# Performance work log

Measured on AMD Instinct MI355X. Metric: run time of the kernel, lower is better.

## Reference

```python
import jax, jax.numpy as jnp
import numpy as np

H, I, B = 256, 128, 512

def setup_inputs() -> dict:
    key = jax.random.key(0)
    ks = jax.random.split(key, 24)
    n = lambda k, shp, s=1.0: jax.random.normal(k, shp, dtype=jnp.float32) * s
    inp = {
        "x": n(ks[0], (B, I)),
        "hx": n(ks[1], (B, H), 0.1),
        "cx": n(ks[2], (B, H, H), 0.1),
        # input->gate weights (hidden, input), xavier-like scale
        "Wii": n(ks[3], (H, I), (2.0 / (H + I)) ** 0.5),
        "Wif": n(ks[4], (H, I), (2.0 / (H + I)) ** 0.5),
        "Wig": n(ks[5], (H, I), (2.0 / (H + I)) ** 0.5),
        "Wio": n(ks[6], (H, I), (2.0 / (H + I)) ** 0.5),
        # hidden->gate weights (hidden, hidden), ~orthogonal scale
        "Whi": n(ks[7], (H, H), H ** -0.5),
        "Whit": n(ks[8], (H, H), H ** -0.5),
        "Whf": n(ks[9], (H, H), H ** -0.5),
        "Whft": n(ks[10], (H, H), H ** -0.5),
        "Whc": n(ks[11], (H, H), H ** -0.5),
        "Whct": n(ks[12], (H, H), H ** -0.5),
        "Who": n(ks[13], (H, H), H ** -0.5),
        "Uinv": n(ks[14], (H, H), H ** -0.5),
        "Vtinv": n(ks[15], (H, H), H ** -0.5),
        # biases: bi/bf/bg are full (H,H) matrices, bo is (H,1)
        "bi": jnp.zeros((H, H), jnp.float32),
        "bf": jnp.zeros((H, H), jnp.float32),
        "bg": jnp.zeros((H, H), jnp.float32),
        "bo": jnp.zeros((H, 1), jnp.float32),
    }
    return inp


def reference(x, hx, cx, Wii, Wif, Wig, Wio, Whi, Whit, Whf, Whft, Whc, Whct, Who, Uinv, Vtinv, bi, bf, bg, bo):
    # W @ diag(v) @ M^T  ==  einsum('hi,bi,gi->bhg', W, v, M)
    def sandwich(Wx, Wh, Wht, b):
        # (Wx*x) @ Wx^T + (Wh*hx) @ Wht^T + b  -> (B,H,H)
        xt = jnp.einsum('hi,bi,gi->bhg', Wx, x, Wx)
        ht = jnp.einsum('hj,bj,gj->bhg', Wh, hx, Wht)
        return xt + ht + b

    i = jax.nn.sigmoid(sandwich(Wii, Whi, Whit, bi))
    f = jax.nn.sigmoid(sandwich(Wif, Whf, Whft, bf))
    g = jnp.tanh(sandwich(Wig, Whc, Whct, bg))
    # o: ordinary vector gate (B,H)
    o = jax.nn.sigmoid(jnp.einsum('hi,bi->bh', Wio, x)
                       + jnp.einsum('hj,bj->bh', Who, hx) + bo[:, 0])
    cx_new = f * cx + i * g                     # (B,H,H)
    # diag(Uinv @ cx_new @ Vtinv) per batch element -> (B,H)
    proj_down = jnp.einsum('ij,bjk,ki->bi', Uinv, cx_new, Vtinv)
    hx_new = o * jax.nn.sigmoid(proj_down)
    return hx_new
```

## Files before the change

### kernel.cpp

```cpp
#include <hip/hip_runtime.h>
#include <hip/hip_bf16.h>

#define Hh 256
#define Ii 128
#define KF 384
#define KB 64
#define BK 64
#define LDSB 72

typedef __attribute__((ext_vector_type(8))) short bf16x8;
typedef __attribute__((ext_vector_type(4))) float f32x4;
typedef unsigned short u16;
typedef unsigned int u32;

__device__ inline float bf2f(u16 u) { return __uint_as_float(((u32)u) << 16); }
__device__ inline u16 f2bf(float f) {
  u32 u = __float_as_uint(f);
  u += 0x7FFFu + ((u >> 16) & 1u);
  return (u16)(u >> 16);
}
__device__ inline u32 pack_bf16x2(float a, float b) {
  __hip_bfloat162 h = __float22bfloat162_rn(make_float2(a, b));
  u32 r; __builtin_memcpy(&r, &h, 4); return r;
}
__device__ inline u32 scale2(u32 packed, float va, float vb) {
  float lo = __uint_as_float(packed << 16) * va;
  float hi = __uint_as_float(packed & 0xFFFF0000u) * vb;
  return pack_bf16x2(lo, hi);
}
__device__ inline float sigm(float x) { return 1.0f / (1.0f + __expf(-x)); }
__device__ inline float tanh_f(float x) { return 1.0f - 2.0f / (1.0f + __expf(2.0f * x)); }

union U32x4 { bf16x8 f; u32 d[4]; uint4 v; };

__global__ __launch_bounds__(256) void k_prep(
    const float* __restrict__ Wii, const float* __restrict__ Wif, const float* __restrict__ Wig,
    const float* __restrict__ Whi, const float* __restrict__ Whit,
    const float* __restrict__ Whf, const float* __restrict__ Whft,
    const float* __restrict__ Whc, const float* __restrict__ Whct,
    const float* __restrict__ Vtinv, const float* __restrict__ Uinv,
    const float* __restrict__ bi, const float* __restrict__ bfm, const float* __restrict__ bg,
    u16* __restrict__ RW, u16* __restrict__ CW, u16* __restrict__ Vtt,
    u16* __restrict__ biasP, float* __restrict__ UinvP, float* __restrict__ proj) {
  const int tid = threadIdx.x, bx = blockIdx.x, y = blockIdx.y;
  if (y < 3) {
    const float* WX  = (y == 0) ? Wii : (y == 1 ? Wif : Wig);
    const float* WHr = (y == 0) ? Whi : (y == 1 ? Whf : Whc);
    const float* WHt = (y == 0) ? Whit : (y == 1 ? Whft : Whct);
    u16* rw = RW + y * Hh * KF;
    u16* cw = CW + y * Hh * KF;
#pragma unroll
    for (int it = 0; it < 4; ++it) {
      int idx = it * 24576 + bx * 256 + tid;
      int h = idx / KF, t = idx - h * KF;
      float a, c;
      if (t < Ii) { a = WX[h * Ii + t]; c = a; }
      else        { a = WHr[h * Hh + t - Ii]; c = WHt[h * Hh + t - Ii]; }
      rw[idx] = f2bf(a);
      cw[idx] = f2bf(c);
    }
  } else if (y == 3) {
    if (bx < 64) {
      __shared__ u16 tbuf[32][33];
      const int c = tid & 31, r8 = tid >> 5;
      const int tr = bx >> 3, tc = bx & 7;
#pragma unroll
      for (int rr = r8; rr < 32; rr += 8)
        tbuf[rr][c] = f2bf(Vtinv[(tc * 32 + rr) * Hh + tr * 32 + c]);
      __syncthreads();
#pragma unroll
      for (int rr = r8; rr < 32; rr += 8)
        Vtt[(tr * 32 + rr) * Hh + tc * 32 + c] = tbuf[c][rr];
    } else if (bx < 96) {
      const int base = (bx - 64) * 256 + tid;
      const float4 z = {0.f, 0.f, 0.f, 0.f};
#pragma unroll
      for (int it = 0; it < 4; ++it)
        *(float4*)(proj + (size_t)(it * 8192 + base) * 4) = z;
    }
  } else if (y == 4) {
    const int base = (bx * 256 + tid) * 8;
#pragma unroll
    for (int e8 = 0; e8 < 8; ++e8) {
      int f = base + e8;
      int ph = f >> 16;
      int r1 = f & 65535;
      int jb = r1 >> 14;
      int r2 = r1 & 16383;
      int kb = r2 >> 12;
      int r3 = r2 & 4095;
      int t  = r3 >> 4;
      int e  = r3 & 15;
      int w = t >> 6, quad = (t >> 4) & 3, r15 = t & 15;
      int tk = e >> 2, rr = e & 3;
      int j   = jb * 64 + w * 16 + quad * 4 + rr;
      int col = kb * 64 + tk * 16 + r15;
      const float* src = (ph == 0) ? bg : (ph == 1 ? bi : bfm);
      biasP[f] = f2bf(src[j * Hh + col]);
    }
  } else {
    if (bx < 32) {
      const int base = (bx * 256 + tid) * 8;
#pragma unroll
      for (int e8 = 0; e8 < 8; ++e8) {
        int f = base + e8;
        int jb = f >> 14;
        int r2 = f & 16383;
        int t  = r2 >> 6;
        int e  = r2 & 63;
        int ti = e >> 4, tj = (e >> 2) & 3, rr = e & 3;
        int w = t >> 6, quad = (t >> 4) & 3, r15 = t & 15;
        int i = w * 64 + ti * 16 + quad * 4 + rr;
        int j = jb * 64 + tj * 16 + r15;
        UinvP[f] = Uinv[i * Hh + j];
      }
    }
  }
}

__global__ __launch_bounds__(256) void k_main(
    const float* __restrict__ x, const float* __restrict__ hx, const float* __restrict__ cx,
    const u16* __restrict__ RW, const u16* __restrict__ CW,
    const u16* __restrict__ Vtt, const u16* __restrict__ biasP,
    const float* __restrict__ UinvP, float* __restrict__ proj) {
  __shared__ u16 sB[2 * KB * LDSB];
  __shared__ u16 sP[KB * LDSB];
  __shared__ float sV[KF];

  const int tid  = threadIdx.x;
  const int b    = blockIdx.x >> 4;
  const int jb   = (blockIdx.x >> 2) & 3;
  const int kb   = blockIdx.x & 3;
  const int k0   = kb * KB;
  const int lane = tid & 63;
  const int w    = tid >> 6;
  const int r15  = lane & 15;
  const int quad = lane >> 4;
  const int jbase = jb * 64 + w * 16;
  const int brow = tid >> 2, bcg = tid & 3;

  if (tid < Ii) sV[tid] = x[b * Ii + tid];
  sV[Ii + tid] = hx[b * Hh + tid];

  const u16* rwp[3] = {RW + 2 * Hh * KF, RW, RW + 1 * Hh * KF};
  const u16* cwp[3] = {CW + 2 * Hh * KF, CW, CW + 1 * Hh * KF};
  const float* cx_b = cx + (size_t)b * Hh * Hh;

  __syncthreads();

  U32x4 n0, n1;
  {
    const u16* src = cwp[0] + (size_t)(k0 + brow) * KF + bcg * 16;
    n0.v = *(const uint4*)src;
    n1.v = *(const uint4*)(src + 8);
  }
  bf16x8 fa[2];
  fa[0] = *(const bf16x8*)(rwp[0] + (size_t)(jbase + r15) * KF + quad * 8);
  fa[1] = *(const bf16x8*)(rwp[0] + (size_t)(jbase + r15) * KF + 32 + quad * 8);
  {
    U32x4 o0, o1;
    const float4 v0 = *(const float4*)(&sV[bcg * 16]);
    const float4 v1 = *(const float4*)(&sV[bcg * 16 + 4]);
    const float4 v2 = *(const float4*)(&sV[bcg * 16 + 8]);
    const float4 v3 = *(const float4*)(&sV[bcg * 16 + 12]);
    o0.d[0] = scale2(n0.d[0], v0.x, v0.y); o0.d[1] = scale2(n0.d[1], v0.z, v0.w);
    o0.d[2] = scale2(n0.d[2], v1.x, v1.y); o0.d[3] = scale2(n0.d[3], v1.z, v1.w);
    o1.d[0] = scale2(n1.d[0], v2.x, v2.y); o1.d[1] = scale2(n1.d[1], v2.z, v2.w);
    o1.d[2] = scale2(n1.d[2], v3.x, v3.y); o1.d[3] = scale2(n1.d[3], v3.z, v3.w);
    u16* dst = sB + brow * LDSB + bcg * 16;
    *(uint4*)dst = o0.v;
    *(uint4*)(dst + 8) = o1.v;
  }
  __syncthreads();

  float p[4][4];

#pragma unroll
  for (int ph = 0; ph < 3; ++ph) {
    f32x4 acc[4];
#pragma unroll
    for (int tk = 0; tk < 4; ++tk)
#pragma unroll
      for (int r = 0; r < 4; ++r) acc[tk][r] = 0.0f;

#pragma unroll
    for (int kc = 0; kc < 6; ++kc) {
      const int sc = ph * 6 + kc;
      const int cur = sc & 1;
      const int nph = (kc < 5) ? ph : (ph < 2 ? ph + 1 : 0);
      const int nt0 = (kc < 5) ? (kc + 1) * BK : 0;
      U32x4 m0, m1;
      bf16x8 fan[2];
      if (sc < 17) {
        const u16* src = cwp[nph] + (size_t)(k0 + brow) * KF + nt0 + bcg * 16;
        m0.v = *(const uint4*)src;
        m1.v = *(const uint4*)(src + 8);
        fan[0] = *(const bf16x8*)(rwp[nph] + (size_t)(jbase + r15) * KF + nt0 + quad * 8);
        fan[1] = *(const bf16x8*)(rwp[nph] + (size_t)(jbase + r15) * KF + nt0 + 32 + quad * 8);
      }
#pragma unroll
      for (int ks = 0; ks < 2; ++ks) {
        bf16x8 fb[4];
#pragma unroll
        for (int tk = 0; tk < 4; ++tk)
          fb[tk] = *(const bf16x8*)(&sB[cur * (KB * LDSB) + (tk * 16 + r15) * LDSB + ks * 32 + quad * 8]);
#pragma unroll
        for (int tk = 0; tk < 4; ++tk)
          acc[tk] = __builtin_amdgcn_mfma_f32_16x16x32_bf16(fa[ks], fb[tk], acc[tk], 0, 0, 0);
      }
      if (sc < 17) {
        U32x4 o0, o1;
        const float4 v0 = *(const float4*)(&sV[nt0 + bcg * 16]);
        const float4 v1 = *(const float4*)(&sV[nt0 + bcg * 16 + 4]);
        const float4 v2 = *(const float4*)(&sV[nt0 + bcg * 16 + 8]);
        const float4 v3 = *(const float4*)(&sV[nt0 + bcg * 16 + 12]);
        o0.d[0] = scale2(m0.d[0], v0.x, v0.y); o0.d[1] = scale2(m0.d[1], v0.z, v0.w);
        o0.d[2] = scale2(m0.d[2], v1.x, v1.y); o0.d[3] = scale2(m0.d[3], v1.z, v1.w);
        o1.d[0] = scale2(m1.d[0], v2.x, v2.y); o1.d[1] = scale2(m1.d[1], v2.z, v2.w);
        o1.d[2] = scale2(m1.d[2], v3.x, v3.y); o1.d[3] = scale2(m1.d[3], v3.z, v3.w);
        u16* dst = sB + (cur ^ 1) * (KB * LDSB) + brow * LDSB + bcg * 16;
        *(uint4*)dst = o0.v;
        *(uint4*)(dst + 8) = o1.v;
        fa[0] = fan[0];
        fa[1] = fan[1];
      }
      if (kc == 5) {
        const u16* bp = biasP + ((size_t)((ph * 4 + jb) * 4 + kb) * 256 + tid) * 16;
        const uint4 b0 = *(const uint4*)bp;
        const uint4 b1 = *(const uint4*)(bp + 8);
        const u32 bw[8] = {b0.x, b0.y, b0.z, b0.w, b1.x, b1.y, b1.z, b1.w};
        if (ph == 2) {
          float cxv[16];
#pragma unroll
          for (int tk = 0; tk < 4; ++tk)
#pragma unroll
            for (int r = 0; r < 4; ++r)
              cxv[tk * 4 + r] = cx_b[(size_t)(jbase + quad * 4 + r) * Hh + k0 + tk * 16 + r15];
#pragma unroll
          for (int tk = 0; tk < 4; ++tk)
#pragma unroll
            for (int r = 0; r < 4; ++r) {
              const int e = tk * 4 + r;
              const float bias = (e & 1) ? __uint_as_float(bw[e >> 1] & 0xFFFF0000u)
                                         : __uint_as_float(bw[e >> 1] << 16);
              const float z = acc[tk][r] + bias;
              const float c = sigm(z) * cxv[e] + p[tk][r];
              sP[(w * 16 + quad * 4 + r) * LDSB + tk * 16 + r15] = f2bf(c);
            }
        } else {
#pragma unroll
          for (int tk = 0; tk < 4; ++tk)
#pragma unroll
            for (int r = 0; r < 4; ++r) {
              const int e = tk * 4 + r;
              const float bias = (e & 1) ? __uint_as_float(bw[e >> 1] & 0xFFFF0000u)
                                         : __uint_as_float(bw[e >> 1] << 16);
              const float z = acc[tk][r] + bias;
              if (ph == 0) p[tk][r] = tanh_f(z);
              else         p[tk][r] *= sigm(z);
            }
        }
      }
      __syncthreads();
    }
  }

  bf16x8 fbp[2][4];
#pragma unroll
  for (int ks = 0; ks < 2; ++ks)
#pragma unroll
    for (int tj = 0; tj < 4; ++tj)
      fbp[ks][tj] = *(const bf16x8*)(&sP[(tj * 16 + r15) * LDSB + ks * 32 + quad * 8]);

  float racc[4][4];
#pragma unroll
  for (int ti = 0; ti < 4; ++ti)
#pragma unroll
    for (int r = 0; r < 4; ++r) racc[ti][r] = 0.0f;

  const float* up = UinvP + ((size_t)jb * 256 + tid) * 64;
#pragma unroll
  for (int ti = 0; ti < 4; ++ti) {
    const bf16x8 va0 = *(const bf16x8*)(Vtt + (size_t)(w * 64 + ti * 16 + r15) * Hh + k0 + quad * 8);
    const bf16x8 va1 = *(const bf16x8*)(Vtt + (size_t)(w * 64 + ti * 16 + r15) * Hh + k0 + 32 + quad * 8);
    f32x4 pacc[4];
#pragma unroll
    for (int tj = 0; tj < 4; ++tj)
#pragma unroll
      for (int r = 0; r < 4; ++r) pacc[tj][r] = 0.0f;
#pragma unroll
    for (int tj = 0; tj < 4; ++tj)
      pacc[tj] = __builtin_amdgcn_mfma_f32_16x16x32_bf16(va0, fbp[0][tj], pacc[tj], 0, 0, 0);
#pragma unroll
    for (int tj = 0; tj < 4; ++tj)
      pacc[tj] = __builtin_amdgcn_mfma_f32_16x16x32_bf16(va1, fbp[1][tj], pacc[tj], 0, 0, 0);
    const float4 u0 = *(const float4*)(up + ti * 16);
    const float4 u1 = *(const float4*)(up + ti * 16 + 4);
    const float4 u2 = *(const float4*)(up + ti * 16 + 8);
    const float4 u3 = *(const float4*)(up + ti * 16 + 12);
    const float uu[16] = {u0.x, u0.y, u0.z, u0.w, u1.x, u1.y, u1.z, u1.w,
                          u2.x, u2.y, u2.z, u2.w, u3.x, u3.y, u3.z, u3.w};
#pragma unroll
    for (int tj = 0; tj < 4; ++tj)
#pragma unroll
      for (int r = 0; r < 4; ++r)
        racc[ti][r] += pacc[tj][r] * uu[tj * 4 + r];
  }

#pragma unroll
  for (int ti = 0; ti < 4; ++ti)
#pragma unroll
    for (int r = 0; r < 4; ++r) {
      float v = racc[ti][r];
      v += __shfl_xor(v, 1);
      v += __shfl_xor(v, 2);
      v += __shfl_xor(v, 4);
      v += __shfl_xor(v, 8);
      if (r15 == 0) atomicAdd(&proj[b * Hh + w * 64 + ti * 16 + quad * 4 + r], v);
    }
}

__global__ __launch_bounds__(256) void k_out(
    const float* __restrict__ x, const float* __restrict__ hx,
    const float* __restrict__ Wio, const float* __restrict__ Who,
    const float* __restrict__ bo, const float* __restrict__ proj,
    float* __restrict__ out) {
  __shared__ float sv[KF];
  const int b = blockIdx.x, tid = threadIdx.x;
  const int lane = tid & 63, w = tid >> 6;
  if (tid < Ii) sv[tid] = x[b * Ii + tid];
  sv[Ii + tid] = hx[b * Hh + tid];
  __syncthreads();
  for (int rr = 0; rr < 64; ++rr) {
    const int h = w * 64 + rr;
    float p = Wio[h * Ii + lane]        * sv[lane]
            + Wio[h * Ii + 64 + lane]   * sv[64 + lane]
            + Who[h * Hh + lane]        * sv[128 + lane]
            + Who[h * Hh + 64 + lane]   * sv[192 + lane]
            + Who[h * Hh + 128 + lane]  * sv[256 + lane]
            + Who[h * Hh + 192 + lane]  * sv[320 + lane];
    p += __shfl_xor(p, 32);
    p += __shfl_xor(p, 16);
    p += __shfl_xor(p, 8);
    p += __shfl_xor(p, 4);
    p += __shfl_xor(p, 2);
    p += __shfl_xor(p, 1);
    if (lane == 0)
      out[b * Hh + h] = sigm(p + bo[h]) * sigm(proj[b * Hh + h]);
  }
}

extern "C" void kernel_launch(void* const* d_in, const int* in_sizes, int n_in,
                              void* d_out, int out_size, void* d_ws, size_t ws_size,
                              hipStream_t stream) {
  (void)in_sizes; (void)n_in; (void)out_size; (void)ws_size;
  const float* x    = (const float*)d_in[0];
  const float* hx   = (const float*)d_in[1];
  const float* cx   = (const float*)d_in[2];
  const float* Wii  = (const float*)d_in[3];
  const float* Wif  = (const float*)d_in[4];
  const float* Wig  = (const float*)d_in[5];
  const float* Wio  = (const float*)d_in[6];
  const float* Whi  = (const float*)d_in[7];
  const float* Whit = (const float*)d_in[8];
  const float* Whf  = (const float*)d_in[9];
  const float* Whft = (const float*)d_in[10];
  const float* Whc  = (const float*)d_in[11];
  const float* Whct = (const float*)d_in[12];
  const float* Who  = (const float*)d_in[13];
  const float* Uinv = (const float*)d_in[14];
  const float* Vtinv= (const float*)d_in[15];
  const float* bi   = (const float*)d_in[16];
  const float* bf   = (const float*)d_in[17];
  const float* bg   = (const float*)d_in[18];
  const float* bo   = (const float*)d_in[19];
  float* out = (float*)d_out;

  u16* RW    = (u16*)d_ws;
  u16* CW    = RW + 3 * Hh * KF;
  u16* Vtt   = CW + 3 * Hh * KF;
  u16* biasP = Vtt + Hh * Hh;
  float* UinvP = (float*)(biasP + 3 * Hh * Hh);
  float* proj  = UinvP + Hh * Hh;

  k_prep<<<dim3(96, 6), 256, 0, stream>>>(Wii, Wif, Wig, Whi, Whit, Whf, Whft, Whc, Whct,
                                          Vtinv, Uinv, bi, bf, bg,
                                          RW, CW, Vtt, biasP, UinvP, proj);
  k_main<<<8192, 256, 0, stream>>>(x, hx, cx, RW, CW, Vtt, biasP, UinvP, proj);
  k_out<<<512, 256, 0, stream>>>(x, hx, Wio, Who, bo, proj, out);
}
```

Measured before the change: 564.1 us.

## Stream CW tiles directly to LDS and scale the A operand instead

The column-weight tile is now loaded with global_load_lds straight into an XOR-swizzled, unpadded LDS buffer, so it no longer goes through registers. The diag(v) scaling moves from the B tile to the per-wave A fragment in registers. The separate sP buffer is dropped and the cell state reuses sB with the same swizzle. This cuts VGPR traffic, LDS footprint and bank conflicts, at the cost of redoing the A-operand scaling in every wave and depending on the async LDS load being visible at the existing barriers.

```diff
diff --git a/kernel.cpp b/kernel.cpp
--- a/kernel.cpp
+++ b/kernel.cpp
@@ -5,8 +5,6 @@
 #define Ii 128
 #define KF 384
 #define KB 64
-#define BK 64
-#define LDSB 72
 
 typedef __attribute__((ext_vector_type(8))) short bf16x8;
 typedef __attribute__((ext_vector_type(4))) float f32x4;
@@ -30,6 +28,12 @@
 }
 __device__ inline float sigm(float x) { return 1.0f / (1.0f + __expf(-x)); }
 __device__ inline float tanh_f(float x) { return 1.0f - 2.0f / (1.0f + __expf(2.0f * x)); }
+
+__device__ __forceinline__ void gld_lds16(const u16* g, u16* l) {
+  __builtin_amdgcn_global_load_lds(
+      (const __attribute__((address_space(1))) u32*)g,
+      (__attribute__((address_space(3))) u32*)l, 16, 0, 0);
+}
 
 union U32x4 { bf16x8 f; u32 d[4]; uint4 v; };
 
@@ -123,8 +127,7 @@
     const u16* __restrict__ RW, const u16* __restrict__ CW,
     const u16* __restrict__ Vtt, const u16* __restrict__ biasP,
     const float* __restrict__ UinvP, float* __restrict__ proj) {
-  __shared__ u16 sB[2 * KB * LDSB];
-  __shared__ u16 sP[KB * LDSB];
+  __shared__ u16 sB[2 * 4096];
   __shared__ float sV[KF];
 
   const int tid  = threadIdx.x;
@@ -137,7 +140,6 @@
   const int r15  = lane & 15;
   const int quad = lane >> 4;
   const int jbase = jb * 64 + w * 16;
-  const int brow = tid >> 2, bcg = tid & 3;
 
   if (tid < Ii) sV[tid] = x[b * Ii + tid];
   sV[Ii + tid] = hx[b * Hh + tid];
@@ -146,38 +148,25 @@
   const u16* cwp[3] = {CW + 2 * Hh * KF, CW, CW + 1 * Hh * KF};
   const float* cx_b = cx + (size_t)b * Hh * Hh;
 
+  const int flat0 = w * 128 + lane;
+  const int row0  = flat0 >> 3, sl0 = flat0 & 7;
+  const int flat1 = flat0 + 64;
+  const int row1  = flat1 >> 3, sl1 = flat1 & 7;
+  const size_t goff0 = (size_t)(k0 + row0) * KF + (sl0 ^ (row0 & 7)) * 8;
+  const size_t goff1 = (size_t)(k0 + row1) * KF + (sl1 ^ (row1 & 7)) * 8;
+
+  gld_lds16(cwp[0] + goff0, sB + w * 1024);
+  gld_lds16(cwp[0] + goff1, sB + w * 1024 + 512);
+  bf16x8 fan[2];
+  fan[0] = *(const bf16x8*)(rwp[0] + (size_t)(jbase + r15) * KF + quad * 8);
+  fan[1] = *(const bf16x8*)(rwp[0] + (size_t)(jbase + r15) * KF + 32 + quad * 8);
   __syncthreads();
 
-  U32x4 n0, n1;
-  {
-    const u16* src = cwp[0] + (size_t)(k0 + brow) * KF + bcg * 16;
-    n0.v = *(const uint4*)src;
-    n1.v = *(const uint4*)(src + 8);
-  }
-  bf16x8 fa[2];
-  fa[0] = *(const bf16x8*)(rwp[0] + (size_t)(jbase + r15) * KF + quad * 8);
-  fa[1] = *(const bf16x8*)(rwp[0] + (size_t)(jbase + r15) * KF + 32 + quad * 8);
-  {
-    U32x4 o0, o1;
-    const float4 v0 = *(const float4*)(&sV[bcg * 16]);
-    const float4 v1 = *(const float4*)(&sV[bcg * 16 + 4]);
-    const float4 v2 = *(const float4*)(&sV[bcg * 16 + 8]);
-    const float4 v3 = *(const float4*)(&sV[bcg * 16 + 12]);
-    o0.d[0] = scale2(n0.d[0], v0.x, v0.y); o0.d[1] = scale2(n0.d[1], v0.z, v0.w);
-    o0.d[2] = scale2(n0.d[2], v1.x, v1.y); o0.d[3] = scale2(n0.d[3], v1.z, v1.w);
-    o1.d[0] = scale2(n1.d[0], v2.x, v2.y); o1.d[1] = scale2(n1.d[1], v2.z, v2.w);
-    o1.d[2] = scale2(n1.d[2], v3.x, v3.y); o1.d[3] = scale2(n1.d[3], v3.z, v3.w);
-    u16* dst = sB + brow * LDSB + bcg * 16;
-    *(uint4*)dst = o0.v;
-    *(uint4*)(dst + 8) = o1.v;
-  }
-  __syncthreads();
-
   float p[4][4];
+  f32x4 acc[4];
 
 #pragma unroll
   for (int ph = 0; ph < 3; ++ph) {
-    f32x4 acc[4];
 #pragma unroll
     for (int tk = 0; tk < 4; ++tk)
 #pragma unroll
@@ -185,45 +174,46 @@
 
 #pragma unroll
     for (int kc = 0; kc < 6; ++kc) {
-      const int sc = ph * 6 + kc;
+      const int sc  = ph * 6 + kc;
       const int cur = sc & 1;
-      const int nph = (kc < 5) ? ph : (ph < 2 ? ph + 1 : 0);
-      const int nt0 = (kc < 5) ? (kc + 1) * BK : 0;
-      U32x4 m0, m1;
-      bf16x8 fan[2];
+      const int tb  = kc * 64;
+      const int nph = (kc < 5) ? ph : ph + 1;
+      const int nt0 = (kc < 5) ? (kc + 1) * 64 : 0;
+
       if (sc < 17) {
-        const u16* src = cwp[nph] + (size_t)(k0 + brow) * KF + nt0 + bcg * 16;
-        m0.v = *(const uint4*)src;
-        m1.v = *(const uint4*)(src + 8);
+        gld_lds16(cwp[nph] + goff0 + nt0, sB + (cur ^ 1) * 4096 + w * 1024);
+        gld_lds16(cwp[nph] + goff1 + nt0, sB + (cur ^ 1) * 4096 + w * 1024 + 512);
+      }
+
+      bf16x8 fa[2];
+#pragma unroll
+      for (int ks = 0; ks < 2; ++ks) {
+        const float4 v0 = *(const float4*)(&sV[tb + ks * 32 + quad * 8]);
+        const float4 v1 = *(const float4*)(&sV[tb + ks * 32 + quad * 8 + 4]);
+        U32x4 a, o;
+        a.f = fan[ks];
+        o.d[0] = scale2(a.d[0], v0.x, v0.y);
+        o.d[1] = scale2(a.d[1], v0.z, v0.w);
+        o.d[2] = scale2(a.d[2], v1.x, v1.y);
+        o.d[3] = scale2(a.d[3], v1.z, v1.w);
+        fa[ks] = o.f;
+      }
+      if (sc < 17) {
         fan[0] = *(const bf16x8*)(rwp[nph] + (size_t)(jbase + r15) * KF + nt0 + quad * 8);
         fan[1] = *(const bf16x8*)(rwp[nph] + (size_t)(jbase + r15) * KF + nt0 + 32 + quad * 8);
       }
+
 #pragma unroll
       for (int ks = 0; ks < 2; ++ks) {
-        bf16x8 fb[4];
-#pragma unroll
-        for (int tk = 0; tk < 4; ++tk)
-          fb[tk] = *(const bf16x8*)(&sB[cur * (KB * LDSB) + (tk * 16 + r15) * LDSB + ks * 32 + quad * 8]);
-#pragma unroll
-        for (int tk = 0; tk < 4; ++tk)
-          acc[tk] = __builtin_amdgcn_mfma_f32_16x16x32_bf16(fa[ks], fb[tk], acc[tk], 0, 0, 0);
-      }
-      if (sc < 17) {
-        U32x4 o0, o1;
-        const float4 v0 = *(const float4*)(&sV[nt0 + bcg * 16]);
-        const float4 v1 = *(const float4*)(&sV[nt0 + bcg * 16 + 4]);
-        const float4 v2 = *(const float4*)(&sV[nt0 + bcg * 16 + 8]);
-        const float4 v3 = *(const float4*)(&sV[nt0 + bcg * 16 + 12]);
-        o0.d[0] = scale2(m0.d[0], v0.x, v0.y); o0.d[1] = scale2(m0.d[1], v0.z, v0.w);
-        o0.d[2] = scale2(m0.d[2], v1.x, v1.y); o0.d[3] = scale2(m0.d[3], v1.z, v1.w);
-        o1.d[0] = scale2(m1.d[0], v2.x, v2.y); o1.d[1] = scale2(m1.d[1], v2.z, v2.w);
-        o1.d[2] = scale2(m1.d[2], v3.x, v3.y); o1.d[3] = scale2(m1.d[3], v3.z, v3.w);
-        u16* dst = sB + (cur ^ 1) * (KB * LDSB) + brow * LDSB + bcg * 16;
-        *(uint4*)dst = o0.v;
-        *(uint4*)(dst + 8) = o1.v;
-        fa[0] = fan[0];
-        fa[1] = fan[1];
-      }
+#pragma unroll
+        for (int tk = 0; tk < 4; ++tk) {
+          const int row = tk * 16 + r15;
+          const int sl  = ((ks * 4 + quad) ^ (r15 & 7)) * 8;
+          const bf16x8 fb = *(const bf16x8*)(&sB[cur * 4096 + row * 64 + sl]);
+          acc[tk] = __builtin_amdgcn_mfma_f32_16x16x32_bf16(fa[ks], fb, acc[tk], 0, 0, 0);
+        }
+      }
+
       if (kc == 5) {
         const u16* bp = biasP + ((size_t)((ph * 4 + jb) * 4 + kb) * 256 + tid) * 16;
         const uint4 b0 = *(const uint4*)bp;
@@ -245,7 +235,10 @@
                                          : __uint_as_float(bw[e >> 1] << 16);
               const float z = acc[tk][r] + bias;
               const float c = sigm(z) * cxv[e] + p[tk][r];
-              sP[(w * 16 + quad * 4 + r) * LDSB + tk * 16 + r15] = f2bf(c);
+              const int jr = w * 16 + quad * 4 + r;
+              const int kk = tk * 16 + r15;
+              const int sl = ((kk >> 3) ^ (jr & 7)) * 8 + (kk & 7);
+              sB[jr * 64 + sl] = f2bf(c);
             }
         } else {
 #pragma unroll
@@ -269,8 +262,11 @@
 #pragma unroll
   for (int ks = 0; ks < 2; ++ks)
 #pragma unroll
-    for (int tj = 0; tj < 4; ++tj)
-      fbp[ks][tj] = *(const bf16x8*)(&sP[(tj * 16 + r15) * LDSB + ks * 32 + quad * 8]);
+    for (int tj = 0; tj < 4; ++tj) {
+      const int j = tj * 16 + r15;
+      const int sl = ((ks * 4 + quad) ^ (j & 7)) * 8;
+      fbp[ks][tj] = *(const bf16x8*)(&sB[j * 64 + sl]);
+    }
 
   float racc[4][4];
 #pragma unroll
@@ -294,17 +290,14 @@
 #pragma unroll
     for (int tj = 0; tj < 4; ++tj)
       pacc[tj] = __builtin_amdgcn_mfma_f32_16x16x32_bf16(va1, fbp[1][tj], pacc[tj], 0, 0, 0);
-    const float4 u0 = *(const float4*)(up + ti * 16);
-    const float4 u1 = *(const float4*)(up + ti * 16 + 4);
-    const float4 u2 = *(const float4*)(up + ti * 16 + 8);
-    const float4 u3 = *(const float4*)(up + ti * 16 + 12);
-    const float uu[16] = {u0.x, u0.y, u0.z, u0.w, u1.x, u1.y, u1.z, u1.w,
-                          u2.x, u2.y, u2.z, u2.w, u3.x, u3.y, u3.z, u3.w};
-#pragma unroll
-    for (int tj = 0; tj < 4; ++tj)
-#pragma unroll
-      for (int r = 0; r < 4; ++r)
-        racc[ti][r] += pacc[tj][r] * uu[tj * 4 + r];
+#pragma unroll
+    for (int tj = 0; tj < 4; ++tj) {
+      const float4 u = *(const float4*)(up + ti * 16 + tj * 4);
+      racc[ti][0] += pacc[tj][0] * u.x;
+      racc[ti][1] += pacc[tj][1] * u.y;
+      racc[ti][2] += pacc[tj][2] * u.z;
+      racc[ti][3] += pacc[tj][3] * u.w;
+    }
   }
 
 #pragma unroll
```

Result: slower. 583.3 us (+3.4%).
